# Kernel optimization log

Measured on AMD Instinct MI355X. Metric: run time of the kernel, lower is better.

Reference implementation:

```python
import jax, jax.numpy as jnp
import numpy as np

N = 50000        # num nodes
E = 1600000      # num edges
D = 128          # hidden_dim
R = 2            # num_relations
L = 2            # num rgcn layers
DES, TWE, NUM, CAT = 768, 768, 5, 6


def _lin_init(key, fan_in, fan_out):
    kw, kb = jax.random.split(key)
    s = 1.0 / np.sqrt(fan_in)
    w = jax.random.uniform(kw, (fan_in, fan_out), jnp.float32, -s, s)
    b = jax.random.uniform(kb, (fan_out,), jnp.float32, -s, s)
    return w, b


def setup_inputs() -> dict:
    key = jax.random.key(0)
    ks = jax.random.split(key, 16)
    des = jax.random.normal(ks[0], (N, DES), jnp.float32)
    tweets = jax.random.normal(ks[1], (N, TWE), jnp.float32)
    num = jax.random.normal(ks[2], (N, NUM), jnp.float32)
    cat = jax.random.normal(ks[3], (N, CAT), jnp.float32)
    edge_index = jax.random.randint(ks[4], (2, E), 0, N, jnp.int64 if jax.config.jax_enable_x64 else jnp.int32)
    edge_type = jax.random.randint(ks[5], (E,), 0, R, edge_index.dtype)

    des_w, des_b = _lin_init(ks[6], DES, D)
    tweet_w, tweet_b = _lin_init(ks[7], TWE, D)
    num_w, num_b = _lin_init(ks[8], NUM, D)
    cat_w, cat_b = _lin_init(ks[9], CAT, D)

    s = 1.0 / np.sqrt(D)
    rel_w = jax.random.uniform(ks[10], (L, R, D, D), jnp.float32, -s, s)   # per-layer per-relation weight
    root_w = jax.random.uniform(ks[11], (L, D, D), jnp.float32, -s, s)     # per-layer root weight
    rgcn_b = jax.random.uniform(ks[12], (L, D), jnp.float32, -s, s)        # per-layer bias

    mlp_w1, mlp_b1 = _lin_init(ks[13], D, D)
    mlp_w2, mlp_b2 = _lin_init(ks[14], D, 2)

    return dict(des=des, tweets=tweets, num=num, cat=cat,
                edge_index=edge_index, edge_type=edge_type,
                des_w=des_w, des_b=des_b, tweet_w=tweet_w, tweet_b=tweet_b,
                num_w=num_w, num_b=num_b, cat_w=cat_w, cat_b=cat_b,
                rel_w=rel_w, root_w=root_w, rgcn_b=rgcn_b,
                mlp_w1=mlp_w1, mlp_b1=mlp_b1, mlp_w2=mlp_w2, mlp_b2=mlp_b2)


def _lrelu(v):
    return jax.nn.leaky_relu(v, 0.01)  # torch F.leaky_relu default slope


def _rgcn_layer(x, edge_index, edge_type, rel_w_l, root_w_l, b_l):
    # PyG RGCNConv with num_bases=None, aggr='mean':
    # out = x @ root + bias + sum_r mean_{j in N_r(i)} x_j @ W_r
    src, dst = edge_index[0], edge_index[1]
    out = x @ root_w_l + b_l
    xs = x[src]  # [E, D] gathered source features
    for r in range(R):
        mask = (edge_type == r).astype(x.dtype)          # [E]
        msg = (xs @ rel_w_l[r]) * mask[:, None]          # [E, D]
        ssum = jax.ops.segment_sum(msg, dst, num_segments=N)           # [N, D]
        cnt = jax.ops.segment_sum(mask, dst, num_segments=N)           # [N]
        out = out + ssum / jnp.maximum(cnt, 1.0)[:, None]
    return out


def reference(des, tweets, num, cat, edge_index, edge_type,
              des_w, des_b, tweet_w, tweet_b, num_w, num_b, cat_w, cat_b,
              rel_w, root_w, rgcn_b, mlp_w1, mlp_b1, mlp_w2, mlp_b2):
    # multi-modal projections, fused leaky-relu + sum (eval mode: no dropout)
    x = (_lrelu(des @ des_w + des_b)
         + _lrelu(tweets @ tweet_w + tweet_b)
         + _lrelu(num @ num_w + num_b)
         + _lrelu(cat @ cat_w + cat_b))
    for l in range(L):
        x = _lrelu(_rgcn_layer(x, edge_index, edge_type, rel_w[l], root_w[l], rgcn_b[l]))
    h = jax.nn.relu(x @ mlp_w1 + mlp_b1)
    return h @ mlp_w2 + mlp_b2  # [N, 2]
```

## Files before the change

### kernel.cpp

```cpp
#include <hip/hip_runtime.h>

#define NN 50000
#define EE 1600000
#define NBINS (2 * NN)
#define SCAN_NB ((NBINS + 255) / 256)

typedef __attribute__((ext_vector_type(8))) short bf16x8;
typedef __attribute__((ext_vector_type(8))) unsigned short u16x8;
typedef __attribute__((ext_vector_type(4))) float f32x4;

__device__ __forceinline__ float bf2f(unsigned short u) {
    union { unsigned int u; float f; } v; v.u = ((unsigned int)u) << 16; return v.f;
}
__device__ __forceinline__ unsigned short f2bf(float f) {
    union { float f; unsigned int u; } v; v.f = f;
    unsigned int x = v.u;
    x += ((x >> 16) & 1u) + 0x7FFFu;
    return (unsigned short)(x >> 16);
}
__device__ __forceinline__ float lrelu(float v) { return (v > 0.f) ? v : 0.01f * v; }

struct TRArgs {
    const float* src[9];
    unsigned short* dhi[9];
    unsigned short* dlo[9];
    int K[9];
    int base[10];
};

__global__ void rg_tr_all(TRArgs a) {
    const int i = blockIdx.x * 256 + threadIdx.x;
    if (i >= a.base[9]) return;
    int s = 0;
    while (s < 8 && i >= a.base[s + 1]) ++s;
    const int j = i - a.base[s];
    const int K = a.K[s];
    const int k = j >> 7;
    const int c = j & 127;
    const float v = a.src[s][j];
    const unsigned short h = f2bf(v);
    a.dhi[s][c * K + k] = h;
    a.dlo[s][c * K + k] = f2bf(v - bf2f(h));
}

__global__ void rg_hist(const int* __restrict__ ei, const int* __restrict__ et,
                        int* __restrict__ hist) {
    int e = blockIdx.x * 256 + threadIdx.x;
    if (e >= EE) return;
    const int dst = ei[EE + e];
    const int r = et[e];
    atomicAdd(&hist[r * NN + dst], 1);
}

__global__ void rg_scan_blk(const int* __restrict__ hist, int* __restrict__ bsum) {
    const int t = threadIdx.x;
    const int idx = blockIdx.x * 256 + t;
    int v = (idx < NBINS) ? hist[idx] : 0;
#pragma unroll
    for (int off = 32; off > 0; off >>= 1) v += __shfl_down(v, off, 64);
    __shared__ int ws[4];
    if ((t & 63) == 0) ws[t >> 6] = v;
    __syncthreads();
    if (t == 0) bsum[blockIdx.x] = ws[0] + ws[1] + ws[2] + ws[3];
}

__global__ void rg_scan_top(const int* __restrict__ bsum, int* __restrict__ boff,
                            int* __restrict__ offs) {
    __shared__ int ls[512];
    const int t = threadIdx.x;
    const int v = (t < SCAN_NB) ? bsum[t] : 0;
    ls[t] = v;
    __syncthreads();
    for (int d = 1; d < 512; d <<= 1) {
        const int u = (t >= d) ? ls[t - d] : 0;
        __syncthreads();
        ls[t] += u;
        __syncthreads();
    }
    if (t < SCAN_NB) boff[t] = ls[t] - v;
    if (t == SCAN_NB - 1) offs[NBINS] = ls[t];
}

__global__ void rg_scan_fin(const int* __restrict__ hist, const int* __restrict__ boff,
                            int* __restrict__ offs, int* __restrict__ cursor) {
    __shared__ int ls[256];
    const int t = threadIdx.x;
    const int idx = blockIdx.x * 256 + t;
    const int v = (idx < NBINS) ? hist[idx] : 0;
    ls[t] = v;
    __syncthreads();
    for (int d = 1; d < 256; d <<= 1) {
        const int u = (t >= d) ? ls[t - d] : 0;
        __syncthreads();
        ls[t] += u;
        __syncthreads();
    }
    if (idx < NBINS) {
        const int o = boff[blockIdx.x] + ls[t] - v;
        offs[idx] = o;
        cursor[idx] = o;
    }
}

__global__ void rg_place(const int* __restrict__ ei, const int* __restrict__ et,
                         int* __restrict__ cursor, int* __restrict__ sorted_src) {
    int e = blockIdx.x * 256 + threadIdx.x;
    if (e >= EE) return;
    const int src = ei[e];
    const int dst = ei[EE + e];
    const int r = et[e];
    const int pos = atomicAdd(&cursor[r * NN + dst], 1);
    sorted_src[pos] = src;
}

__global__ void rg_gather(const float* __restrict__ xf,
                          const int* __restrict__ sorted_src,
                          const int* __restrict__ offs,
                          float* __restrict__ agg) {
    const int lane = threadIdx.x & 63;
    const int half = lane >> 5;
    const int l32 = lane & 31;
    const int gw = (blockIdx.x * blockDim.x + threadIdx.x) >> 6;
    const int nw = (gridDim.x * blockDim.x) >> 6;
    for (int bin = gw; bin < NBINS; bin += nw) {
        const int s = offs[bin], e = offs[bin + 1];
        f32x4 a0 = (f32x4){0.f, 0.f, 0.f, 0.f};
        f32x4 a1 = (f32x4){0.f, 0.f, 0.f, 0.f};
        int i = s;
        for (; i + 3 < e; i += 4) {
            const int r0 = sorted_src[i + half];
            const int r1 = sorted_src[i + 2 + half];
            const f32x4 v0 = *(const f32x4*)(xf + (long)r0 * 128 + l32 * 4);
            const f32x4 v1 = *(const f32x4*)(xf + (long)r1 * 128 + l32 * 4);
            a0 += v0;
            a1 += v1;
        }
        for (; i < e; i += 2) {
            const int idx = i + half;
            if (idx < e) {
                const int r0 = sorted_src[idx];
                a0 += *(const f32x4*)(xf + (long)r0 * 128 + l32 * 4);
            }
        }
        a0 += a1;
#pragma unroll
        for (int j = 0; j < 4; ++j) a0[j] += __shfl_xor(a0[j], 32, 64);
        if (half == 0) {
            const float c = fmaxf((float)(e - s), 1.0f);
            f32x4 o;
#pragma unroll
            for (int j = 0; j < 4; ++j) o[j] = a0[j] / c;
            *(f32x4*)(agg + (long)bin * 128 + l32 * 4) = o;
        }
    }
}

__global__ __launch_bounds__(256) void rg_part(
    const float* __restrict__ A0, const float* __restrict__ A1,
    const float* __restrict__ A2,
    const unsigned short* __restrict__ BH0, const unsigned short* __restrict__ BH1,
    const unsigned short* __restrict__ BH2,
    const unsigned short* __restrict__ BL0, const unsigned short* __restrict__ BL1,
    const unsigned short* __restrict__ BL2,
    float* __restrict__ O0, float* __restrict__ O1, float* __restrict__ O2,
    int kb0, int kb1, int kb2,
    int ks0, int ks1, int ks2,
    int Kstr, int bps)
{
    __shared__ unsigned short Ahi[64 * 40];
    __shared__ unsigned short Alo[64 * 40];
    __shared__ unsigned short Bhi[128 * 40];
    __shared__ unsigned short Blo[128 * 40];

    const int seg = blockIdx.x / bps;
    const int blk = blockIdx.x - seg * bps;

    const float* A;
    const unsigned short* BH;
    const unsigned short* BL;
    float* O;
    int kbase, ksteps;
    if (seg == 0)      { A = A0; BH = BH0; BL = BL0; O = O0; kbase = kb0; ksteps = ks0; }
    else if (seg == 1) { A = A1; BH = BH1; BL = BL1; O = O1; kbase = kb1; ksteps = ks1; }
    else               { A = A2; BH = BH2; BL = BL2; O = O2; kbase = kb2; ksteps = ks2; }

    const int tid = threadIdx.x;
    const int wave = tid >> 6, lane = tid & 63, q = lane >> 4, m15 = lane & 15;
    const int row0 = blk * 64;
    const int ar = tid >> 2, aseg = tid & 3;
    const int bn = tid >> 1, bb = (tid & 1) * 16;
    const int agr = row0 + ar;
    const bool aval = agr < NN;

    f32x4 acc[8];
#pragma unroll
    for (int t = 0; t < 8; ++t) acc[t] = (f32x4){0.f, 0.f, 0.f, 0.f};

    for (int ks = 0; ks < ksteps; ++ks) {
        const int k0 = kbase + (ks << 5);
        __syncthreads();
        {
            u16x8 hi = {0,0,0,0,0,0,0,0}, lo = {0,0,0,0,0,0,0,0};
            if (aval) {
                const float* p = A + (long)agr * Kstr + k0 + aseg * 8;
                const f32x4 v0 = *(const f32x4*)p;
                const f32x4 v1 = *(const f32x4*)(p + 4);
#pragma unroll
                for (int j = 0; j < 4; ++j) {
                    unsigned short h0 = f2bf(v0[j]);
                    hi[j] = h0;  lo[j] = f2bf(v0[j] - bf2f(h0));
                    unsigned short h1 = f2bf(v1[j]);
                    hi[j+4] = h1; lo[j+4] = f2bf(v1[j] - bf2f(h1));
                }
            }
            *(u16x8*)(Ahi + ar * 40 + aseg * 8) = hi;
            *(u16x8*)(Alo + ar * 40 + aseg * 8) = lo;
        }
        {
            const long bo = (long)bn * Kstr + k0 + bb;
            *(u16x8*)(Bhi + bn * 40 + bb)     = *(const u16x8*)(BH + bo);
            *(u16x8*)(Bhi + bn * 40 + bb + 8) = *(const u16x8*)(BH + bo + 8);
            *(u16x8*)(Blo + bn * 40 + bb)     = *(const u16x8*)(BL + bo);
            *(u16x8*)(Blo + bn * 40 + bb + 8) = *(const u16x8*)(BL + bo + 8);
        }
        __syncthreads();
        const bf16x8 ah = *(const bf16x8*)(Ahi + (wave * 16 + m15) * 40 + q * 8);
        const bf16x8 al = *(const bf16x8*)(Alo + (wave * 16 + m15) * 40 + q * 8);
#pragma unroll
        for (int t = 0; t < 8; ++t) {
            const bf16x8 bh = *(const bf16x8*)(Bhi + ((t << 4) + m15) * 40 + q * 8);
            const bf16x8 bl = *(const bf16x8*)(Blo + ((t << 4) + m15) * 40 + q * 8);
            acc[t] = __builtin_amdgcn_mfma_f32_16x16x32_bf16(ah, bh, acc[t], 0, 0, 0);
            acc[t] = __builtin_amdgcn_mfma_f32_16x16x32_bf16(al, bh, acc[t], 0, 0, 0);
            acc[t] = __builtin_amdgcn_mfma_f32_16x16x32_bf16(ah, bl, acc[t], 0, 0, 0);
        }
    }
#pragma unroll
    for (int t = 0; t < 8; ++t) {
        const int col = (t << 4) + m15;
#pragma unroll
        for (int i = 0; i < 4; ++i) {
            const int r = row0 + wave * 16 + q * 4 + i;
            if (r < NN) O[(long)r * 128 + col] = acc[t][i];
        }
    }
}

__global__ void rg_proj_fin(
    const float* __restrict__ Ptwe,
    const float* __restrict__ Pd0, const float* __restrict__ Pd1,
    const float* __restrict__ numf, const float* __restrict__ catf,
    const float* __restrict__ num_w, const float* __restrict__ cat_w,
    const float* __restrict__ desB, const float* __restrict__ tweB,
    const float* __restrict__ numB, const float* __restrict__ catB,
    float* __restrict__ xf)
{
    const int lane = threadIdx.x & 63;
    const int gw = (blockIdx.x * blockDim.x + threadIdx.x) >> 6;
    const int nw = (gridDim.x * blockDim.x) >> 6;
    const int c = lane * 2;

    float wn0[5], wn1[5], wc0[6], wc1[6];
#pragma unroll
    for (int k = 0; k < 5; ++k) { wn0[k] = num_w[k * 128 + c]; wn1[k] = num_w[k * 128 + c + 1]; }
#pragma unroll
    for (int k = 0; k < 6; ++k) { wc0[k] = cat_w[k * 128 + c]; wc1[k] = cat_w[k * 128 + c + 1]; }
    const float bn0 = numB[c], bn1 = numB[c + 1];
    const float bc0 = catB[c], bc1 = catB[c + 1];
    const float bd0 = desB[c], bd1 = desB[c + 1];
    const float bt0 = tweB[c], bt1 = tweB[c + 1];

    for (int n = gw; n < NN; n += nw) {
        const long o = (long)n * 128 + c;
        const float2 tw = *(const float2*)(Ptwe + o);
        const float2 d0 = *(const float2*)(Pd0 + o);
        const float2 d1 = *(const float2*)(Pd1 + o);
        float nv[5], cv[6];
#pragma unroll
        for (int k = 0; k < 5; ++k) nv[k] = numf[(long)n * 5 + k];
#pragma unroll
        for (int k = 0; k < 6; ++k) cv[k] = catf[(long)n * 6 + k];
        float s1x = bn0, s1y = bn1;
#pragma unroll
        for (int k = 0; k < 5; ++k) { s1x += nv[k] * wn0[k]; s1y += nv[k] * wn1[k]; }
        float s2x = bc0, s2y = bc1;
#pragma unroll
        for (int k = 0; k < 6; ++k) { s2x += cv[k] * wc0[k]; s2y += cv[k] * wc1[k]; }
        const float rx = lrelu(tw.x + bt0) + lrelu(d0.x + d1.x + bd0)
                       + lrelu(s1x) + lrelu(s2x);
        const float ry = lrelu(tw.y + bt1) + lrelu(d0.y + d1.y + bd1)
                       + lrelu(s1y) + lrelu(s2y);
        *(float2*)(xf + o) = make_float2(rx, ry);
    }
}

__global__ __launch_bounds__(256) void rg_gemm(
    const float* __restrict__ A0, const float* __restrict__ A1,
    const float* __restrict__ A2,
    const unsigned short* __restrict__ B0h, const unsigned short* __restrict__ B0l,
    const unsigned short* __restrict__ B1h, const unsigned short* __restrict__ B1l,
    const unsigned short* __restrict__ B2h, const unsigned short* __restrict__ B2l,
    const float* __restrict__ bias, int S, int act,
    float* __restrict__ outf)
{
    __shared__ unsigned short Ahi[64 * 40];
    __shared__ unsigned short Alo[64 * 40];
    __shared__ unsigned short Bhi[128 * 40];
    __shared__ unsigned short Blo[128 * 40];

    const int tid = threadIdx.x;
    const int wave = tid >> 6, lane = tid & 63, q = lane >> 4, m15 = lane & 15;
    const int row0 = blockIdx.x * 64;

    const float* Aptr[3] = { A0, A1, A2 };
    const unsigned short* BHptr[3] = { B0h, B1h, B2h };
    const unsigned short* BLptr[3] = { B0l, B1l, B2l };

    f32x4 acc[8];
#pragma unroll
    for (int t = 0; t < 8; ++t) acc[t] = (f32x4){0.f, 0.f, 0.f, 0.f};

    for (int s = 0; s < S; ++s) {
        const float* A = Aptr[s];
        const unsigned short* BH = BHptr[s];
        const unsigned short* BL = BLptr[s];
#pragma unroll
        for (int ks = 0; ks < 4; ++ks) {
            const int k0 = ks << 5;
            __syncthreads();
            {
                const int r = tid >> 2, seg = tid & 3;
                const int gr = row0 + r;
                u16x8 hi = {0,0,0,0,0,0,0,0}, lo = {0,0,0,0,0,0,0,0};
                if (gr < NN) {
                    const float* p = A + (long)gr * 128 + k0 + seg * 8;
                    const f32x4 v0 = *(const f32x4*)p;
                    const f32x4 v1 = *(const f32x4*)(p + 4);
#pragma unroll
                    for (int j = 0; j < 4; ++j) {
                        unsigned short h0 = f2bf(v0[j]);
                        hi[j] = h0;  lo[j] = f2bf(v0[j] - bf2f(h0));
                        unsigned short h1 = f2bf(v1[j]);
                        hi[j+4] = h1; lo[j+4] = f2bf(v1[j] - bf2f(h1));
                    }
                }
                *(u16x8*)(Ahi + r * 40 + seg * 8) = hi;
                *(u16x8*)(Alo + r * 40 + seg * 8) = lo;
            }
            {
                const int n = tid >> 1;
                const int base = (tid & 1) * 16;
                *(u16x8*)(Bhi + n * 40 + base)     = *(const u16x8*)(BH + (long)n * 128 + k0 + base);
                *(u16x8*)(Bhi + n * 40 + base + 8) = *(const u16x8*)(BH + (long)n * 128 + k0 + base + 8);
                *(u16x8*)(Blo + n * 40 + base)     = *(const u16x8*)(BL + (long)n * 128 + k0 + base);
                *(u16x8*)(Blo + n * 40 + base + 8) = *(const u16x8*)(BL + (long)n * 128 + k0 + base + 8);
            }
            __syncthreads();
            const bf16x8 ah = *(const bf16x8*)(Ahi + (wave * 16 + m15) * 40 + q * 8);
            const bf16x8 al = *(const bf16x8*)(Alo + (wave * 16 + m15) * 40 + q * 8);
#pragma unroll
            for (int t = 0; t < 8; ++t) {
                const bf16x8 bh = *(const bf16x8*)(Bhi + ((t << 4) + m15) * 40 + q * 8);
                const bf16x8 bl = *(const bf16x8*)(Blo + ((t << 4) + m15) * 40 + q * 8);
                acc[t] = __builtin_amdgcn_mfma_f32_16x16x32_bf16(ah, bh, acc[t], 0, 0, 0);
                acc[t] = __builtin_amdgcn_mfma_f32_16x16x32_bf16(al, bh, acc[t], 0, 0, 0);
                acc[t] = __builtin_amdgcn_mfma_f32_16x16x32_bf16(ah, bl, acc[t], 0, 0, 0);
            }
        }
    }
#pragma unroll
    for (int t = 0; t < 8; ++t) {
        const int col = (t << 4) + m15;
        const float bv = bias[col];
#pragma unroll
        for (int i = 0; i < 4; ++i) {
            const int r = row0 + wave * 16 + q * 4 + i;
            if (r < NN) {
                float v = acc[t][i] + bv;
                v = act ? fmaxf(v, 0.f) : ((v > 0.f) ? v : 0.01f * v);
                outf[(long)r * 128 + col] = v;
            }
        }
    }
}

__global__ void BotRGCN_64381559767213_kernel(const float* __restrict__ hf,
                                              const float* __restrict__ w2,
                                              const float* __restrict__ b2,
                                              float* __restrict__ out)
{
    const int lane = threadIdx.x & 63;
    const int gw = (blockIdx.x * blockDim.x + threadIdx.x) >> 6;
    const int nw = (gridDim.x * blockDim.x) >> 6;
    const int k2 = lane * 2;
    const float w00 = w2[k2 * 2 + 0], w01 = w2[k2 * 2 + 1];
    const float w10 = w2[k2 * 2 + 2], w11 = w2[k2 * 2 + 3];
    const float b0 = b2[0], b1 = b2[1];
    for (int n = gw; n < NN; n += nw) {
        const float2 v = *(const float2*)(hf + (long)n * 128 + k2);
        float p0 = v.x * w00 + v.y * w10;
        float p1 = v.x * w01 + v.y * w11;
#pragma unroll
        for (int off = 32; off > 0; off >>= 1) {
            p0 += __shfl_down(p0, off, 64);
            p1 += __shfl_down(p1, off, 64);
        }
        if (lane == 0) {
            *(float2*)(out + (long)n * 2) = make_float2(p0 + b0, p1 + b1);
        }
    }
}

extern "C" void kernel_launch(void* const* d_in, const int* in_sizes, int n_in,
                              void* d_out, int out_size, void* d_ws, size_t ws_size,
                              hipStream_t stream)
{
    const float* des    = (const float*)d_in[0];
    const float* twe    = (const float*)d_in[1];
    const float* num    = (const float*)d_in[2];
    const float* cat    = (const float*)d_in[3];
    const int*   ei     = (const int*)d_in[4];
    const int*   et     = (const int*)d_in[5];
    const float* des_w  = (const float*)d_in[6];
    const float* des_b  = (const float*)d_in[7];
    const float* twe_w  = (const float*)d_in[8];
    const float* twe_b  = (const float*)d_in[9];
    const float* num_w  = (const float*)d_in[10];
    const float* num_b  = (const float*)d_in[11];
    const float* cat_w  = (const float*)d_in[12];
    const float* cat_b  = (const float*)d_in[13];
    const float* rel_w  = (const float*)d_in[14];
    const float* root_w = (const float*)d_in[15];
    const float* rgcn_b = (const float*)d_in[16];
    const float* mlp_w1 = (const float*)d_in[17];
    const float* mlp_b1 = (const float*)d_in[18];
    const float* mlp_w2 = (const float*)d_in[19];
    const float* mlp_b2 = (const float*)d_in[20];

    char* ws = (char*)d_ws;
    size_t off = 0;
    auto alloc = [&](size_t bytes) -> char* {
        char* p = ws + off;
        off += (bytes + 255) & ~(size_t)255;
        return p;
    };
    float* xf  = (float*)alloc((size_t)NN * 128 * 4);
    float* agg = (float*)alloc((size_t)NBINS * 128 * 4);
    int* hist       = (int*)alloc((size_t)NBINS * 4);
    int* offs       = (int*)alloc((size_t)(NBINS + 1) * 4);
    int* cursor     = (int*)alloc((size_t)NBINS * 4);
    int* sorted_src = (int*)alloc((size_t)EE * 4);
    int* bsum       = (int*)alloc((size_t)SCAN_NB * 4);
    int* boff       = (int*)alloc((size_t)SCAN_NB * 4);
    unsigned short* desHi = (unsigned short*)alloc((size_t)768 * 128 * 2);
    unsigned short* desLo = (unsigned short*)alloc((size_t)768 * 128 * 2);
    unsigned short* tweHi = (unsigned short*)alloc((size_t)768 * 128 * 2);
    unsigned short* tweLo = (unsigned short*)alloc((size_t)768 * 128 * 2);
    unsigned short* rootHi = (unsigned short*)alloc((size_t)2 * 16384 * 2);
    unsigned short* rootLo = (unsigned short*)alloc((size_t)2 * 16384 * 2);
    unsigned short* relHi  = (unsigned short*)alloc((size_t)4 * 16384 * 2);
    unsigned short* relLo  = (unsigned short*)alloc((size_t)4 * 16384 * 2);
    unsigned short* w1Hi   = (unsigned short*)alloc((size_t)16384 * 2);
    unsigned short* w1Lo   = (unsigned short*)alloc((size_t)16384 * 2);
    float* hf = agg;

    {
        TRArgs a;
        const float* srcs[9] = { des_w, twe_w, root_w, root_w + 16384,
                                 rel_w, rel_w + 16384, rel_w + 2 * 16384, rel_w + 3 * 16384,
                                 mlp_w1 };
        unsigned short* his[9] = { desHi, tweHi, rootHi, rootHi + 16384,
                                   relHi, relHi + 16384, relHi + 2 * 16384, relHi + 3 * 16384,
                                   w1Hi };
        unsigned short* los[9] = { desLo, tweLo, rootLo, rootLo + 16384,
                                   relLo, relLo + 16384, relLo + 2 * 16384, relLo + 3 * 16384,
                                   w1Lo };
        const int Ks[9] = { 768, 768, 128, 128, 128, 128, 128, 128, 128 };
        int b = 0;
        for (int s = 0; s < 9; ++s) {
            a.src[s] = srcs[s]; a.dhi[s] = his[s]; a.dlo[s] = los[s]; a.K[s] = Ks[s];
            a.base[s] = b; b += Ks[s] * 128;
        }
        a.base[9] = b;
        rg_tr_all<<<(b + 255) / 256, 256, 0, stream>>>(a);
    }

    hipMemsetAsync(hist, 0, (size_t)NBINS * 4, stream);
    rg_hist<<<(EE + 255) / 256, 256, 0, stream>>>(ei, et, hist);
    rg_scan_blk<<<SCAN_NB, 256, 0, stream>>>(hist, bsum);
    rg_scan_top<<<1, 512, 0, stream>>>(bsum, boff, offs);
    rg_scan_fin<<<SCAN_NB, 256, 0, stream>>>(hist, boff, offs, cursor);
    rg_place<<<(EE + 255) / 256, 256, 0, stream>>>(ei, et, cursor, sorted_src);

    const int bps = (NN + 63) / 64;

    rg_part<<<3 * bps, 256, 0, stream>>>(
        twe, des, des,
        tweHi, desHi, desHi,
        tweLo, desLo, desLo,
        xf, agg, agg + (size_t)NN * 128,
        0, 0, 384,
        24, 12, 12,
        768, bps);
    rg_proj_fin<<<2048, 256, 0, stream>>>(xf, agg, agg + (size_t)NN * 128,
                                          num, cat, num_w, cat_w,
                                          des_b, twe_b, num_b, cat_b, xf);

    const int gather_grid = (NBINS * 64 + 255) / 256;
    for (int l = 0; l < 2; ++l) {
        rg_gather<<<gather_grid, 256, 0, stream>>>(xf, sorted_src, offs, agg);
        rg_gemm<<<bps, 256, 0, stream>>>(
            xf, agg, agg + (size_t)NN * 128,
            rootHi + (size_t)l * 16384, rootLo + (size_t)l * 16384,
            relHi + (size_t)(l * 2) * 16384, relLo + (size_t)(l * 2) * 16384,
            relHi + (size_t)(l * 2 + 1) * 16384, relLo + (size_t)(l * 2 + 1) * 16384,
            rgcn_b + l * 128, 3, 0, xf);
    }
    rg_gemm<<<bps, 256, 0, stream>>>(xf, nullptr, nullptr,
                                     w1Hi, w1Lo, nullptr, nullptr, nullptr, nullptr,
                                     mlp_b1, 1, 1, hf);
    BotRGCN_64381559767213_kernel<<<2048, 256, 0, stream>>>(hf, mlp_w2, mlp_b2,
                                                            (float*)d_out);
}
```

Before: 914.8 us.

## Split RGCN layer GEMM into parallel partial products plus a fused epilogue kernel

Each RGCN layer's fused three-operand GEMM (root plus two relation terms) is replaced by the existing rg_part kernel. That kernel runs the three products as separate block groups, each writing its partial result in place over its input buffer. A new elementwise kernel then sums the three partials, adds the bias and applies leaky ReLU. The aim is to triple the block count for better occupancy, at the cost of extra global-memory traffic for the partials and one more launch. Separately, the neighbor gather loop is unrolled to eight edges with four accumulators, to put more independent loads in flight.

Result: slower. 948.3 us (+3.7%).

```diff
diff --git a/kernel.cpp b/kernel.cpp
--- a/kernel.cpp
+++ b/kernel.cpp
@@ -126,14 +126,18 @@
         const int s = offs[bin], e = offs[bin + 1];
         f32x4 a0 = (f32x4){0.f, 0.f, 0.f, 0.f};
         f32x4 a1 = (f32x4){0.f, 0.f, 0.f, 0.f};
+        f32x4 a2 = (f32x4){0.f, 0.f, 0.f, 0.f};
+        f32x4 a3 = (f32x4){0.f, 0.f, 0.f, 0.f};
         int i = s;
-        for (; i + 3 < e; i += 4) {
+        for (; i + 7 < e; i += 8) {
             const int r0 = sorted_src[i + half];
             const int r1 = sorted_src[i + 2 + half];
-            const f32x4 v0 = *(const f32x4*)(xf + (long)r0 * 128 + l32 * 4);
-            const f32x4 v1 = *(const f32x4*)(xf + (long)r1 * 128 + l32 * 4);
-            a0 += v0;
-            a1 += v1;
+            const int r2 = sorted_src[i + 4 + half];
+            const int r3 = sorted_src[i + 6 + half];
+            a0 += *(const f32x4*)(xf + (long)r0 * 128 + l32 * 4);
+            a1 += *(const f32x4*)(xf + (long)r1 * 128 + l32 * 4);
+            a2 += *(const f32x4*)(xf + (long)r2 * 128 + l32 * 4);
+            a3 += *(const f32x4*)(xf + (long)r3 * 128 + l32 * 4);
         }
         for (; i < e; i += 2) {
             const int idx = i + half;
@@ -142,7 +146,7 @@
                 a0 += *(const f32x4*)(xf + (long)r0 * 128 + l32 * 4);
             }
         }
-        a0 += a1;
+        a0 = (a0 + a1) + (a2 + a3);
 #pragma unroll
         for (int j = 0; j < 4; ++j) a0[j] += __shfl_xor(a0[j], 32, 64);
         if (half == 0) {
@@ -291,6 +295,23 @@
         const float ry = lrelu(tw.y + bt1) + lrelu(d0.y + d1.y + bd1)
                        + lrelu(s1y) + lrelu(s2y);
         *(float2*)(xf + o) = make_float2(rx, ry);
+    }
+}
+
+__global__ void rg_fin3(const float* __restrict__ P0, const float* __restrict__ P1,
+                        const float* __restrict__ P2, const float* __restrict__ bias,
+                        float* __restrict__ out)
+{
+    const int tot = NN * 32;
+    for (int i = blockIdx.x * 256 + threadIdx.x; i < tot; i += gridDim.x * 256) {
+        f32x4 v = ((const f32x4*)P0)[i];
+        v = v + ((const f32x4*)P1)[i];
+        v = v + ((const f32x4*)P2)[i];
+        const f32x4 b = *(const f32x4*)(bias + ((i & 31) << 2));
+        v = v + b;
+#pragma unroll
+        for (int j = 0; j < 4; ++j) v[j] = lrelu(v[j]);
+        ((f32x4*)out)[i] = v;
     }
 }
 
@@ -509,13 +530,22 @@
     const int gather_grid = (NBINS * 64 + 255) / 256;
     for (int l = 0; l < 2; ++l) {
         rg_gather<<<gather_grid, 256, 0, stream>>>(xf, sorted_src, offs, agg);
-        rg_gemm<<<bps, 256, 0, stream>>>(
+        rg_part<<<3 * bps, 256, 0, stream>>>(
             xf, agg, agg + (size_t)NN * 128,
-            rootHi + (size_t)l * 16384, rootLo + (size_t)l * 16384,
-            relHi + (size_t)(l * 2) * 16384, relLo + (size_t)(l * 2) * 16384,
-            relHi + (size_t)(l * 2 + 1) * 16384, relLo + (size_t)(l * 2 + 1) * 16384,
-            rgcn_b + l * 128, 3, 0, xf);
-    }
+            rootHi + (size_t)l * 16384,
+            relHi + (size_t)(l * 2) * 16384,
+            relHi + (size_t)(l * 2 + 1) * 16384,
+            rootLo + (size_t)l * 16384,
+            relLo + (size_t)(l * 2) * 16384,
+            relLo + (size_t)(l * 2 + 1) * 16384,
+            xf, agg, agg + (size_t)NN * 128,
+            0, 0, 0,
+            4, 4, 4,
+            128, bps);
+        rg_fin3<<<2048, 256, 0, stream>>>(xf, agg, agg + (size_t)NN * 128,
+                                          rgcn_b + l * 128, xf);
+    }
+
     rg_gemm<<<bps, 256, 0, stream>>>(xf, nullptr, nullptr,
                                      w1Hi, w1Lo, nullptr, nullptr, nullptr, nullptr,
                                      mlp_b1, 1, 1, hf);
```
